# Optimization experiments

Measured on AMD Instinct MI355X. Metric: run time of the kernel, lower is better.

## Reference

```python
import jax, jax.numpy as jnp
import numpy as np

DIM = 256
N_STATE = 8
DT_RANK = 16  # ceil(dim/16)
D_CONV = 4
HIDDEN = 128  # dim * rank_ratio
EPS = 1e-6


def rmsnorm(x, w):
    # matches torch: x / (||x||_2 / sqrt(d) + eps) * w
    norm = jnp.sqrt(jnp.sum(x * x, axis=-1, keepdims=True))
    return x / (norm / np.sqrt(x.shape[-1]) + EPS) * w


def dwconv1d(x, w, b, pad_l, pad_r):
    # x: (b, l, c); w: (c, 1, k) depthwise
    out = jax.lax.conv_general_dilated(
        x.transpose(0, 2, 1), w, window_strides=(1,),
        padding=[(pad_l, pad_r)], dimension_numbers=('NCH', 'OIH', 'NCH'),
        feature_group_count=w.shape[0])
    return (out + b[None, :, None]).transpose(0, 2, 1)


def selective_scan(x, delta, A, Bm, Cm, D):
    # x, delta: (b,l,d); A: (d,n); Bm, Cm: (b,l,n); D: (d,)
    dA = jnp.exp(delta[..., None] * A)                     # (b,l,d,n)
    dBx = (delta * x)[..., None] * Bm[:, :, None, :]       # (b,l,d,n)

    def step(h, inp):
        dA_t, dBx_t, C_t = inp
        h = dA_t * h + dBx_t                               # (b,d,n)
        y = jnp.einsum('bdn,bn->bd', h, C_t)
        return h, y

    h0 = jnp.zeros((x.shape[0],) + A.shape, dtype=x.dtype)
    _, ys = jax.lax.scan(step, h0,
                         (dA.transpose(1, 0, 2, 3), dBx.transpose(1, 0, 2, 3),
                          Cm.transpose(1, 0, 2)))
    return ys.transpose(1, 0, 2) + x * D                   # (b,l,d)


def mamba_branch(x, ctx, conv_w, conv_b, xproj_w, dtproj_w, dtproj_b, A_log, D):
    xc = jax.nn.silu(dwconv1d(x, conv_w, conv_b, D_CONV - 1, 0))  # causal conv
    x_dbl = ctx @ xproj_w.T                                  # (b,l,r+2n)
    dt, Bm, Cm = jnp.split(x_dbl, [DT_RANK, DT_RANK + N_STATE], axis=-1)
    delta = jax.nn.softplus(dt @ dtproj_w.T + dtproj_b)
    A = -jnp.exp(A_log)
    return selective_scan(xc, delta, A, Bm, Cm, D)


def setup_inputs() -> dict:
    key = jax.random.key(0)
    ks = jax.random.split(key, 24)
    B, L, D = 4, 64 * 64, DIM
    s = 0.02
    A_log_init = jnp.log(jnp.broadcast_to(jnp.arange(1, N_STATE + 1, dtype=jnp.float32), (D, N_STATE)))
    dt_bias = jnp.full((D,), jnp.log(jnp.expm1(0.01)), dtype=jnp.float32)
    inp = {
        'x0': jax.random.normal(ks[0], (B, L, D), jnp.float32),
        'x1': jax.random.normal(ks[1], (B, L, D), jnp.float32),
        'w_norm0': jnp.ones((D,), jnp.float32),
        'w_norm1': jnp.ones((D,), jnp.float32),
        'in_proj_w': jax.random.normal(ks[2], (2 * D, D), jnp.float32) * s,
        'conv_w_f': jax.random.normal(ks[3], (D, 1, D_CONV), jnp.float32) * 0.3,
        'conv_b_f': jnp.zeros((D,), jnp.float32),
        'xproj_w_f': jax.random.normal(ks[4], (DT_RANK + 2 * N_STATE, D), jnp.float32) * s,
        'dtproj_w_f': jax.random.normal(ks[5], (D, DT_RANK), jnp.float32) * 0.1,
        'dtproj_b_f': dt_bias,
        'A_log_f': A_log_init,
        'D_f': jnp.ones((D,), jnp.float32),
        'conv_w_bw': jax.random.normal(ks[6], (D, 1, D_CONV), jnp.float32) * 0.3,
        'conv_b_bw': jnp.zeros((D,), jnp.float32),
        'xproj_w_bw': jax.random.normal(ks[7], (DT_RANK + 2 * N_STATE, D), jnp.float32) * s,
        'dtproj_w_bw': jax.random.normal(ks[8], (D, DT_RANK), jnp.float32) * 0.1,
        'dtproj_b_bw': dt_bias,
        'A_log_bw': A_log_init,
        'D_bw': jnp.ones((D,), jnp.float32),
        'norm_y_w': jnp.ones((D,), jnp.float32),
        'out_proj_w': jax.random.normal(ks[9], (D, D), jnp.float32) * s,
        'fc1_w': jax.random.normal(ks[10], (HIDDEN, D), jnp.float32) * s,
        'dw_w': jax.random.normal(ks[11], (HIDDEN, 1, 3), jnp.float32) * 0.3,
        'dw_b': jnp.zeros((HIDDEN,), jnp.float32),
        'fc2_w': jax.random.normal(ks[12], (D, HIDDEN), jnp.float32) * s,
    }
    return inp


def reference(x0, x1, w_norm0, w_norm1, in_proj_w, conv_w_f, conv_b_f, xproj_w_f,
              dtproj_w_f, dtproj_b_f, A_log_f, D_f, conv_w_bw, conv_b_bw,
              xproj_w_bw, dtproj_w_bw, dtproj_b_bw, A_log_bw, D_bw, norm_y_w,
              out_proj_w, fc1_w, dw_w, dw_b, fc2_w):
    residual = x0
    h0 = rmsnorm(x0, w_norm0)
    h1 = rmsnorm(x1, w_norm1)
    # cross-Mamba: main stream x0 -> x,z; extra_emb x1 -> dt/B/C
    xz = h0 @ in_proj_w.T
    xin, z = jnp.split(xz, 2, axis=-1)
    y_f = mamba_branch(xin, h1, conv_w_f, conv_b_f, xproj_w_f, dtproj_w_f,
                       dtproj_b_f, A_log_f, D_f)
    y_b = jnp.flip(mamba_branch(jnp.flip(xin, 1), jnp.flip(h1, 1), conv_w_bw,
                                conv_b_bw, xproj_w_bw, dtproj_w_bw, dtproj_b_bw,
                                A_log_bw, D_bw), 1)
    y = (y_f + y_b) * 0.5          # if_devide_out=True (bidirectional)
    y = rmsnorm(y, norm_y_w)       # use_norm=True
    y = y * jax.nn.silu(z)
    x = y @ out_proj_w.T + residual
    # LowRankFeedForward (dropout = identity at eval)
    m = x @ fc1_w.T
    m = jax.nn.silu(dwconv1d(m, dw_w, dw_b, 1, 1))
    m = m @ fc2_w.T
    return x + m
```

## Files before the change

kernel.cpp:

```cpp
#include <hip/hip_runtime.h>
#include <math.h>
#include <cstddef>

#define BB 4
#define LL 4096
#define DD 256
#define NST 8
#define RANK 16
#define HID 128
#define BL (BB*LL)
#define BLD ((size_t)BL*DD)
#define CH 256
#define CLEN 16
#define XZS 512

typedef __bf16 bf16x8 __attribute__((ext_vector_type(8)));
typedef float  f32x4  __attribute__((ext_vector_type(4)));

__device__ __forceinline__ float siluf(float x){ return x / (1.f + __expf(-x)); }
__device__ __forceinline__ float softplus_fast(float x){
  float r = __logf(1.f + __expf(x));
  return x > 15.f ? x : r;
}
__device__ __forceinline__ unsigned short f2bf(float x){
  union { float f; unsigned u; } v; v.f = x;
  unsigned r = v.u + 0x7fffu + ((v.u >> 16) & 1u);
  return (unsigned short)(r >> 16);
}
__device__ __forceinline__ float bf2f(unsigned short u){
  union { unsigned u32; float f; } c; c.u32 = ((unsigned)u) << 16;
  return c.f;
}

__global__ __launch_bounds__(64) void rms_kernel(
    const float* __restrict__ x0, const float* __restrict__ w0, unsigned short* __restrict__ o0b,
    const float* __restrict__ x1, const float* __restrict__ w1, unsigned short* __restrict__ o1b)
{
  const float* x; const float* w; unsigned short* o;
  if (blockIdx.y == 0){ x = x0; w = w0; o = o0b; } else { x = x1; w = w1; o = o1b; }
  size_t tok = blockIdx.x;
  int lane = threadIdx.x;
  float4 v = ((const float4*)(x + tok*DD))[lane];
  float s = v.x*v.x + v.y*v.y + v.z*v.z + v.w*v.w;
  #pragma unroll
  for (int m = 1; m < 64; m <<= 1) s += __shfl_xor(s, m, 64);
  float scale = 1.f / (sqrtf(s) * (1.f/16.f) + 1e-6f);
  float4 wv = ((const float4*)w)[lane];
  ushort4 r;
  r.x = f2bf(v.x*scale*wv.x); r.y = f2bf(v.y*scale*wv.y);
  r.z = f2bf(v.z*scale*wv.z); r.w = f2bf(v.w*scale*wv.w);
  ((ushort4*)(o + tok*DD))[lane] = r;
}

__global__ __launch_bounds__(256) void cvt1_kernel(
    const float* __restrict__ s, unsigned short* __restrict__ d, int n)
{
  int i = blockIdx.x*256 + threadIdx.x;
  if (i < n) d[i] = f2bf(s[i]);
}
__global__ __launch_bounds__(256) void cvt5_kernel(
    const float* __restrict__ s0, const float* __restrict__ s1,
    const float* __restrict__ s2, const float* __restrict__ s3,
    const float* __restrict__ s4, unsigned short* __restrict__ d)
{
  int i = blockIdx.x*256 + threadIdx.x;
  if (i >= 147456) return;
  float v;
  if (i < 8192)        v = s0[i];
  else if (i < 16384)  v = s1[i - 8192];
  else if (i < 81920)  v = s2[i - 16384];
  else if (i < 114688) v = s3[i - 81920];
  else                 v = s4[i - 114688];
  d[i] = f2bf(v);
}

template<int EPI>
__global__ __launch_bounds__(256) void gemm_mfma(
    const unsigned short* __restrict__ A, const unsigned short* __restrict__ Bw,
    float* __restrict__ C, const float* __restrict__ Add,
    unsigned short* __restrict__ Cb, int M, int ldc, int K)
{
  constexpr int BK = 64, PAD = 8;
  __shared__ __align__(16) unsigned short As[64][BK+PAD];
  __shared__ __align__(16) unsigned short Bs[64][BK+PAD];
  int tid  = threadIdx.x;
  int row0 = blockIdx.x * 64;
  int col0 = blockIdx.y * 64;
  int wave = tid >> 6, lane = tid & 63;
  int wm = (wave >> 1) * 32, wn = (wave & 1) * 32;
  int lm = lane & 15, kq = lane >> 4;
  int sr = tid >> 2, sc16 = (tid & 3) * 16;

  f32x4 acc[2][2];
  #pragma unroll
  for (int i = 0; i < 2; i++)
    #pragma unroll
    for (int j = 0; j < 2; j++) acc[i][j] = (f32x4){0.f,0.f,0.f,0.f};

  for (int k0 = 0; k0 < K; k0 += BK){
    const unsigned short* ap = &A [(size_t)(row0 + sr)*K + k0 + sc16];
    const unsigned short* bp = &Bw[(size_t)(col0 + sr)*K + k0 + sc16];
    *(int4*)&As[sr][sc16]   = *(const int4*)ap;
    *(int4*)&As[sr][sc16+8] = *(const int4*)(ap + 8);
    *(int4*)&Bs[sr][sc16]   = *(const int4*)bp;
    *(int4*)&Bs[sr][sc16+8] = *(const int4*)(bp + 8);
    __syncthreads();
    #pragma unroll
    for (int ks = 0; ks < 2; ks++){
      bf16x8 af[2], bfv[2];
      #pragma unroll
      for (int i = 0; i < 2; i++) af[i]  = *(const bf16x8*)&As[wm + i*16 + lm][ks*32 + kq*8];
      #pragma unroll
      for (int j = 0; j < 2; j++) bfv[j] = *(const bf16x8*)&Bs[wn + j*16 + lm][ks*32 + kq*8];
      #pragma unroll
      for (int i = 0; i < 2; i++)
        #pragma unroll
        for (int j = 0; j < 2; j++)
          acc[i][j] = __builtin_amdgcn_mfma_f32_16x16x32_bf16(af[i], bfv[j], acc[i][j], 0, 0, 0);
    }
    __syncthreads();
  }

  #pragma unroll
  for (int i = 0; i < 2; i++){
    int rbase = row0 + wm + i*16 + kq*4;
    #pragma unroll
    for (int j = 0; j < 2; j++){
      int col = col0 + wn + j*16 + lm;
      #pragma unroll
      for (int r = 0; r < 4; r++){
        size_t idx = (size_t)(rbase + r)*ldc + col;
        float v = acc[i][j][r];
        if constexpr (EPI == 1 || EPI == 2) v += Add[idx];
        if constexpr (EPI != 3) C[idx] = v;
        if constexpr (EPI == 1 || EPI == 3) Cb[idx] = f2bf(v);
      }
    }
  }
}

__global__ __launch_bounds__(256) void front_kernel(
    const unsigned short* __restrict__ xz,
    const float* __restrict__ xd,
    const float* __restrict__ cwf, const float* __restrict__ cbf,
    const float* __restrict__ cwb, const float* __restrict__ cbb,
    const float* __restrict__ dtwf, const float* __restrict__ dtbf,
    const float* __restrict__ dtwb, const float* __restrict__ dtbb,
    const float* __restrict__ Alogf, const float* __restrict__ Alogb,
    const float* __restrict__ Dfp, const float* __restrict__ Dbp,
    unsigned int* __restrict__ xde,
    float* __restrict__ Sp, float* __restrict__ Hout)
{
  int chunk = blockIdx.x, b = blockIdx.y, dir = blockIdx.z;
  int s0 = chunk*CLEN;
  int d  = threadIdx.x;

  __shared__ float sdt[CLEN][16];
  __shared__ float sB [CLEN][8];
  __shared__ float sC [CLEN][8];
  #pragma unroll
  for (int e = threadIdx.x; e < CLEN*32; e += 256){
    int lt = e >> 5, col = e & 31;
    int pos = s0 + lt;
    int row = dir ? (LL-1-pos) : pos;
    float v = xd[((size_t)b*LL + row)*64 + dir*32 + col];
    if (col < 16)      sdt[lt][col]    = v;
    else if (col < 24) sB [lt][col-16] = v;
    else               sC [lt][col-24] = v;
  }
  __syncthreads();

  float4 cw = ((const float4*)(dir ? cwb : cwf))[d];
  float cb  = (dir ? cbb : cbf)[d];
  const float* dtw = (dir ? dtwb : dtwf) + d*RANK;
  float4 w0 = ((const float4*)dtw)[0], w1 = ((const float4*)dtw)[1];
  float4 w2 = ((const float4*)dtw)[2], w3 = ((const float4*)dtw)[3];
  float dtb = (dir ? dtbb : dtbf)[d];
  float Dd  = (dir ? Dbp : Dfp)[d];

  const unsigned short* xp = xz + (size_t)b*LL*XZS + d;
  #define LDX(pos) ((pos) >= 0 ? bf2f(xp[(size_t)(dir ? (LL-1-(pos)) : (pos))*XZS]) : 0.f)

  float xv[CLEN+3];
  xv[0] = LDX(s0-3); xv[1] = LDX(s0-2); xv[2] = LDX(s0-1);
  #pragma unroll
  for (int i = 0; i < CLEN; i++) xv[3+i] = LDX(s0+i);
  #undef LDX

  unsigned packX[CLEN];
  #pragma unroll
  for (int i = 0; i < CLEN; i++){
    float xc = cb;
    xc = fmaf(cw.x, xv[i],   xc); xc = fmaf(cw.y, xv[i+1], xc);
    xc = fmaf(cw.z, xv[i+2], xc); xc = fmaf(cw.w, xv[i+3], xc);
    xc = siluf(xc);
    const float* dt = &sdt[i][0];
    float de = dtb;
    de = fmaf(dt[0],w0.x, fmaf(dt[1],w0.y, fmaf(dt[2],w0.z, fmaf(dt[3],w0.w, de))));
    de = fmaf(dt[4],w1.x, fmaf(dt[5],w1.y, fmaf(dt[6],w1.z, fmaf(dt[7],w1.w, de))));
    de = fmaf(dt[8],w2.x, fmaf(dt[9],w2.y, fmaf(dt[10],w2.z, fmaf(dt[11],w2.w, de))));
    de = fmaf(dt[12],w3.x, fmaf(dt[13],w3.y, fmaf(dt[14],w3.z, fmaf(dt[15],w3.w, de))));
    de = softplus_fast(de);
    packX[i] = (unsigned)f2bf(xc) | ((unsigned)f2bf(de) << 16);
  }

  const float* Alog = dir ? Alogb : Alogf;
  float A[NST];
  bool fast = true;
  #pragma unroll
  for (int n = 0; n < NST; n++){
    A[n] = -__expf(Alog[d*NST + n]);
    fast = fast && (fabsf(A[n] + (float)(n+1)) < 1e-3f);
  }
  float h[NST];
  #pragma unroll
  for (int n = 0; n < NST; n++) h[n] = 0.f;
  float S = 0.f;

  unsigned int* xout = xde + ((size_t)(dir*BB + b)*LL + s0)*DD + d;

  if (fast){
    #pragma unroll
    for (int t = 0; t < CLEN; t++){
      unsigned pk = packX[t];
      float xc = bf2f((unsigned short)(pk & 0xffffu));
      float de = bf2f((unsigned short)(pk >> 16));
      S += de;
      float dux = de * xc;
      const float* Bv = &sB[t][0];
      const float* Cv = &sC[t][0];
      float e1 = __expf(-de);
      float e2 = e1*e1, e3 = e2*e1, e4 = e2*e2;
      float e5 = e4*e1, e6 = e4*e2, e7 = e4*e3, e8 = e4*e4;
      float acc = xc * Dd;
      h[0] = fmaf(e1, h[0], dux*Bv[0]); acc = fmaf(h[0], Cv[0], acc);
      h[1] = fmaf(e2, h[1], dux*Bv[1]); acc = fmaf(h[1], Cv[1], acc);
      h[2] = fmaf(e3, h[2], dux*Bv[2]); acc = fmaf(h[2], Cv[2], acc);
      h[3] = fmaf(e4, h[3], dux*Bv[3]); acc = fmaf(h[3], Cv[3], acc);
      h[4] = fmaf(e5, h[4], dux*Bv[4]); acc = fmaf(h[4], Cv[4], acc);
      h[5] = fmaf(e6, h[5], dux*Bv[5]); acc = fmaf(h[5], Cv[5], acc);
      h[6] = fmaf(e7, h[6], dux*Bv[6]); acc = fmaf(h[6], Cv[6], acc);
      h[7] = fmaf(e8, h[7], dux*Bv[7]); acc = fmaf(h[7], Cv[7], acc);
      xout[(size_t)t*DD] = (pk & 0xffff0000u) | (unsigned)f2bf(acc);
    }
  } else {
    #pragma unroll
    for (int t = 0; t < CLEN; t++){
      unsigned pk = packX[t];
      float xc = bf2f((unsigned short)(pk & 0xffffu));
      float de = bf2f((unsigned short)(pk >> 16));
      S += de;
      float dux = de * xc;
      const float* Bv = &sB[t][0];
      const float* Cv = &sC[t][0];
      float acc = xc * Dd;
      #pragma unroll
      for (int n = 0; n < NST; n++){
        h[n] = fmaf(__expf(de*A[n]), h[n], dux*Bv[n]);
        acc = fmaf(h[n], Cv[n], acc);
      }
      xout[(size_t)t*DD] = (pk & 0xffff0000u) | (unsigned)f2bf(acc);
    }
  }

  size_t ob = ((((size_t)dir*CH + chunk)*BB + b)*DD + d)*NST;
  float4 h0v, h1v;
  h0v.x=h[0]; h0v.y=h[1]; h0v.z=h[2]; h0v.w=h[3];
  h1v.x=h[4]; h1v.y=h[5]; h1v.z=h[6]; h1v.w=h[7];
  *(float4*)&Hout[ob]   = h0v; *(float4*)&Hout[ob+4] = h1v;
  Sp[((size_t)(dir*CH + chunk)*BB + b)*DD + d] = S;
}

__global__ __launch_bounds__(64) void scan_p2(
    const float* __restrict__ Sp, float* H,
    const float* __restrict__ Alogf, const float* __restrict__ Alogb)
{
  const int SEGC = CH/8;
  int blk = blockIdx.x;
  int d   = blk & (DD-1);
  int b   = (blk >> 8) & (BB-1);
  int dir = blk >> 10;
  int t   = threadIdx.x;
  int seg = t >> 3, n = t & 7;
  float A = -__expf((dir ? Alogb : Alogf)[d*NST + n]);

  const size_t sstr = (size_t)BB*DD;
  const size_t hstr = (size_t)BB*DD*NST;
  size_t sb = (size_t)dir*CH*sstr + (size_t)b*DD + d;
  size_t hb = (size_t)dir*CH*hstr + ((size_t)b*DD + d)*NST + n;
  int c0 = seg*SEGC;

  float pv[SEGC], hv[SEGC];
  #pragma unroll
  for (int k = 0; k < SEGC; k++){
    pv[k] = Sp[sb + (size_t)(c0+k)*sstr];
    hv[k] = H [hb + (size_t)(c0+k)*hstr];
  }
  float h = 0.f, Ss = 0.f;
  #pragma unroll
  for (int k = 0; k < SEGC; k++){
    Ss += pv[k];
    pv[k] = __expf(pv[k]*A);
    h = fmaf(pv[k], h, hv[k]);
  }
  float pi = __expf(Ss*A), hi = h;
  #pragma unroll
  for (int off = 8; off < 64; off <<= 1){
    float hprev = __shfl_up(hi, off, 64);
    float pprev = __shfl_up(pi, off, 64);
    if (t >= off){ hi = fmaf(pi, hprev, hi); pi *= pprev; }
  }
  float hin = __shfl_up(hi, 8, 64);
  h = (seg == 0) ? 0.f : hin;
  #pragma unroll
  for (int k = 0; k < SEGC; k++){
    size_t idx = hb + (size_t)(c0+k)*hstr;
    H[idx] = h;
    h = fmaf(pv[k], h, hv[k]);
  }
}

__global__ __launch_bounds__(256) void back_kernel(
    const unsigned int* __restrict__ xde,
    const float* __restrict__ xd,
    const float* __restrict__ Alogf, const float* __restrict__ Alogb,
    const float* __restrict__ Hin,
    const unsigned short* __restrict__ xz,
    const float* __restrict__ wn,
    unsigned short* __restrict__ outb)
{
  int c  = blockIdx.x, b = blockIdx.y;
  int cbk = CH-1-c;
  int d  = threadIdx.x;
  int T0 = c*CLEN;
  int Pb = cbk*CLEN;

  __shared__ float sCf[CLEN][8], sCb[CLEN][8];
  __shared__ float red[CLEN][4];
  __shared__ float sscale[CLEN];
  {
    int k  = threadIdx.x & 7;
    int lt = (threadIdx.x >> 3) & 15;
    if (threadIdx.x < 128)
      sCf[lt][k] = xd[((size_t)b*LL + T0 + lt)*64 + 24 + k];
    else
      sCb[lt][k] = xd[((size_t)b*LL + (T0 + 15 - lt))*64 + 56 + k];
  }
  __syncthreads();

  float Af[NST], Ab[NST];
  bool fast = true;
  #pragma unroll
  for (int n = 0; n < NST; n++){
    Af[n] = -__expf(Alogf[d*NST + n]);
    Ab[n] = -__expf(Alogb[d*NST + n]);
    fast = fast && (fabsf(Af[n] + (float)(n+1)) < 1e-3f)
                && (fabsf(Ab[n] + (float)(n+1)) < 1e-3f);
  }

  float vf[CLEN];

  {
    float hn[NST];
    size_t ib = (((size_t)c*BB + b)*DD + d)*NST;
    float4 a0 = *(const float4*)&Hin[ib];
    float4 a1 = *(const float4*)&Hin[ib+4];
    hn[0]=a0.x; hn[1]=a0.y; hn[2]=a0.z; hn[3]=a0.w;
    hn[4]=a1.x; hn[5]=a1.y; hn[6]=a1.z; hn[7]=a1.w;
    const unsigned int* p = xde + ((size_t)b*LL + T0)*DD + d;
    unsigned int pk[CLEN];
    #pragma unroll
    for (int t = 0; t < CLEN; t++) pk[t] = p[(size_t)t*DD];
    float S = 0.f;
    if (fast){
      #pragma unroll
      for (int t = 0; t < CLEN; t++){
        float y0 = bf2f((unsigned short)(pk[t] & 0xffffu));
        float de = bf2f((unsigned short)(pk[t] >> 16));
        S += de;
        float E1 = __expf(-S);
        float E2 = E1*E1, E3 = E2*E1, E4 = E2*E2;
        float E5 = E4*E1, E6 = E4*E2, E7 = E4*E3, E8 = E4*E4;
        float corr =      E1 * (hn[0]*sCf[t][0]);
        corr = fmaf(E2, hn[1]*sCf[t][1], corr);
        corr = fmaf(E3, hn[2]*sCf[t][2], corr);
        corr = fmaf(E4, hn[3]*sCf[t][3], corr);
        corr = fmaf(E5, hn[4]*sCf[t][4], corr);
        corr = fmaf(E6, hn[5]*sCf[t][5], corr);
        corr = fmaf(E7, hn[6]*sCf[t][6], corr);
        corr = fmaf(E8, hn[7]*sCf[t][7], corr);
        vf[t] = y0 + corr;
      }
    } else {
      #pragma unroll
      for (int t = 0; t < CLEN; t++){
        float y0 = bf2f((unsigned short)(pk[t] & 0xffffu));
        float de = bf2f((unsigned short)(pk[t] >> 16));
        S += de;
        float corr = 0.f;
        #pragma unroll
        for (int n = 0; n < NST; n++)
          corr = fmaf(__expf(S*Af[n]), hn[n]*sCf[t][n], corr);
        vf[t] = y0 + corr;
      }
    }
  }

  {
    float hn[NST];
    size_t ib = ((((size_t)CH + cbk)*BB + b)*DD + d)*NST;
    float4 a0 = *(const float4*)&Hin[ib];
    float4 a1 = *(const float4*)&Hin[ib+4];
    hn[0]=a0.x; hn[1]=a0.y; hn[2]=a0.z; hn[3]=a0.w;
    hn[4]=a1.x; hn[5]=a1.y; hn[6]=a1.z; hn[7]=a1.w;
    const unsigned int* p = xde + ((size_t)(BB + b)*LL + Pb)*DD + d;
    unsigned int pk[CLEN];
    #pragma unroll
    for (int t = 0; t < CLEN; t++) pk[t] = p[(size_t)t*DD];
    float S = 0.f;
    if (fast){
      #pragma unroll
      for (int t = 0; t < CLEN; t++){
        float y0 = bf2f((unsigned short)(pk[t] & 0xffffu));
        float de = bf2f((unsigned short)(pk[t] >> 16));
        S += de;
        float E1 = __expf(-S);
        float E2 = E1*E1, E3 = E2*E1, E4 = E2*E2;
        float E5 = E4*E1, E6 = E4*E2, E7 = E4*E3, E8 = E4*E4;
        float corr =      E1 * (hn[0]*sCb[t][0]);
        corr = fmaf(E2, hn[1]*sCb[t][1], corr);
        corr = fmaf(E3, hn[2]*sCb[t][2], corr);
        corr = fmaf(E4, hn[3]*sCb[t][3], corr);
        corr = fmaf(E5, hn[4]*sCb[t][4], corr);
        corr = fmaf(E6, hn[5]*sCb[t][5], corr);
        corr = fmaf(E7, hn[6]*sCb[t][6], corr);
        corr = fmaf(E8, hn[7]*sCb[t][7], corr);
        int j = 15 - t;
        vf[j] = 0.5f*(vf[j] + y0 + corr);
      }
    } else {
      #pragma unroll
      for (int t = 0; t < CLEN; t++){
        float y0 = bf2f((unsigned short)(pk[t] & 0xffffu));
        float de = bf2f((unsigned short)(pk[t] >> 16));
        S += de;
        float corr = 0.f;
        #pragma unroll
        for (int n = 0; n < NST; n++)
          corr = fmaf(__expf(S*Ab[n]), hn[n]*sCb[t][n], corr);
        int j = 15 - t;
        vf[j] = 0.5f*(vf[j] + y0 + corr);
      }
    }
  }

  int wave = d >> 6, lane = d & 63;
  #pragma unroll
  for (int j = 0; j < CLEN; j++){
    float s = vf[j]*vf[j];
    #pragma unroll
    for (int m = 1; m < 64; m <<= 1) s += __shfl_xor(s, m, 64);
    if (lane == 0) red[j][wave] = s;
  }
  __syncthreads();
  if (d < CLEN){
    float s = red[d][0] + red[d][1] + red[d][2] + red[d][3];
    sscale[d] = 1.f / (sqrtf(s)*(1.f/16.f) + 1e-6f);
  }
  __syncthreads();

  float wd = wn[d];
  #pragma unroll
  for (int j = 0; j < CLEN; j++){
    size_t tok = (size_t)b*LL + T0 + j;
    float z = bf2f(xz[tok*XZS + 256 + d]);
    outb[tok*DD + d] = f2bf(vf[j]*sscale[j]*wd*siluf(z));
  }
}

__global__ __launch_bounds__(256) void dwconv3_kernel(
    const float* __restrict__ m, const float* __restrict__ w,
    const float* __restrict__ bi, unsigned short* __restrict__ o)
{
  size_t gid = (size_t)blockIdx.x*256 + threadIdx.x;
  int c = (int)(gid % HID);
  int tok = (int)(gid / HID);
  int b = tok / LL, t = tok % LL;
  float acc = bi[c];
  #pragma unroll
  for (int k = 0; k < 3; k++){
    int tt = t - 1 + k;
    if (tt >= 0 && tt < LL)
      acc = fmaf(w[c*3 + k], m[((size_t)b*LL + tt)*HID + c], acc);
  }
  o[gid] = f2bf(siluf(acc));
}

extern "C" void kernel_launch(void* const* d_in, const int* in_sizes, int n_in,
                              void* d_out, int out_size, void* d_ws, size_t ws_size,
                              hipStream_t stream)
{
  const float* x0        = (const float*)d_in[0];
  const float* x1        = (const float*)d_in[1];
  const float* w_norm0   = (const float*)d_in[2];
  const float* w_norm1   = (const float*)d_in[3];
  const float* in_proj_w = (const float*)d_in[4];
  const float* conv_w_f  = (const float*)d_in[5];
  const float* conv_b_f  = (const float*)d_in[6];
  const float* xproj_w_f = (const float*)d_in[7];
  const float* dtproj_w_f= (const float*)d_in[8];
  const float* dtproj_b_f= (const float*)d_in[9];
  const float* A_log_f   = (const float*)d_in[10];
  const float* D_f       = (const float*)d_in[11];
  const float* conv_w_bw = (const float*)d_in[12];
  const float* conv_b_bw = (const float*)d_in[13];
  const float* xproj_w_bw= (const float*)d_in[14];
  const float* dtproj_w_bw=(const float*)d_in[15];
  const float* dtproj_b_bw=(const float*)d_in[16];
  const float* A_log_bw  = (const float*)d_in[17];
  const float* D_bw      = (const float*)d_in[18];
  const float* norm_y_w  = (const float*)d_in[19];
  const float* out_proj_w= (const float*)d_in[20];
  const float* fc1_w     = (const float*)d_in[21];
  const float* dw_w      = (const float*)d_in[22];
  const float* dw_b      = (const float*)d_in[23];
  const float* fc2_w     = (const float*)d_in[24];
  float* out = (float*)d_out;
  float* ws  = (float*)d_ws;

  float* r0 = ws + 0*BLD;
  float* r1 = ws + 1*BLD;
  float* r2 = ws + 2*BLD;
  float* r3 = ws + 3*BLD;
  float* r4 = ws + 4*BLD;
  float* r5 = ws + 5*BLD;
  float* r6 = ws + 6*BLD;
  float* r7 = ws + 7*BLD;

  unsigned short* h0b   = (unsigned short*)r0;
  unsigned short* h1b   = (unsigned short*)r1;
  unsigned short* xz_b  = (unsigned short*)r2;
  float*          xd    = r3;
  unsigned int*   xde   = (unsigned int*)r4;
  unsigned short* wbuf1 = (unsigned short*)r6;
  float* Hout = r6;
  float* Hin  = Hout;
  const size_t SPLANE = (size_t)2*CH*BB*DD;
  float* Sp   = r7 + (BLD - SPLANE);
  unsigned short* ycomb_b = (unsigned short*)r0;
  unsigned short* wbuf2   = (unsigned short*)r7;
  unsigned short* wb_xp   = wbuf2;
  unsigned short* wb_out  = wbuf2 + 16384;
  unsigned short* wb_fc1  = wbuf2 + 81920;
  unsigned short* wb_fc2  = wbuf2 + 114688;
  unsigned short* xb      = wbuf2 + 147456;
  float*          m1      = r4;
  unsigned short* m2b     = (unsigned short*)r5;

  cvt1_kernel<<<dim3(512), 256, 0, stream>>>(in_proj_w, wbuf1, 131072);
  cvt5_kernel<<<dim3(576), 256, 0, stream>>>(
      xproj_w_f, xproj_w_bw, out_proj_w, fc1_w, fc2_w, wbuf2);

  rms_kernel<<<dim3(BL,2), 64, 0, stream>>>(x0, w_norm0, h0b, x1, w_norm1, h1b);

  gemm_mfma<3><<<dim3(BL/64, 8), 256, 0, stream>>>(
      h0b, wbuf1, nullptr, nullptr, xz_b, BL, XZS, 256);

  gemm_mfma<0><<<dim3(BL/64, 1), 256, 0, stream>>>(
      h1b, wb_xp, xd, nullptr, nullptr, BL, 64, 256);

  front_kernel<<<dim3(CH, BB, 2), 256, 0, stream>>>(
      xz_b, xd, conv_w_f, conv_b_f, conv_w_bw, conv_b_bw,
      dtproj_w_f, dtproj_b_f, dtproj_w_bw, dtproj_b_bw,
      A_log_f, A_log_bw, D_f, D_bw, xde, Sp, Hout);

  scan_p2<<<dim3(2*BB*DD), 64, 0, stream>>>(Sp, Hout, A_log_f, A_log_bw);

  back_kernel<<<dim3(CH, BB), 256, 0, stream>>>(
      xde, xd, A_log_f, A_log_bw, Hin, xz_b, norm_y_w, ycomb_b);

  gemm_mfma<1><<<dim3(BL/64, 4), 256, 0, stream>>>(
      ycomb_b, wb_out, out, x0, xb, BL, 256, 256);

  gemm_mfma<0><<<dim3(BL/64, 2), 256, 0, stream>>>(
      xb, wb_fc1, m1, nullptr, nullptr, BL, 128, 256);

  dwconv3_kernel<<<dim3((BL*HID)/256), 256, 0, stream>>>(m1, dw_w, dw_b, m2b);

  gemm_mfma<2><<<dim3(BL/64, 4), 256, 0, stream>>>(
      m2b, wb_fc2, out, out, nullptr, BL, 256, 128);
}
```

Before: 272.2 us.

## Merge weight conversion kernels, vectorize dwconv3, use running products for decay powers

Folds the two weight-conversion launches into one kernel to drop a launch. Vectorizes the depthwise conv3 kernel so each thread handles four channels, using float4 loads and ushort4 stores. Rewrites the decay-power computations in the scan kernels as a serial running product instead of a shallow product tree. The serial chain lengthens the dependency path in the scan's inner loops.

```diff
diff --git a/kernel.cpp b/kernel.cpp
--- a/kernel.cpp
+++ b/kernel.cpp
@@ -52,26 +52,24 @@
   ((ushort4*)(o + tok*DD))[lane] = r;
 }
 
-__global__ __launch_bounds__(256) void cvt1_kernel(
-    const float* __restrict__ s, unsigned short* __restrict__ d, int n)
-{
-  int i = blockIdx.x*256 + threadIdx.x;
-  if (i < n) d[i] = f2bf(s[i]);
-}
-__global__ __launch_bounds__(256) void cvt5_kernel(
+__global__ __launch_bounds__(256) void cvt_kernel(
+    const float* __restrict__ sA,
     const float* __restrict__ s0, const float* __restrict__ s1,
     const float* __restrict__ s2, const float* __restrict__ s3,
-    const float* __restrict__ s4, unsigned short* __restrict__ d)
+    const float* __restrict__ s4,
+    unsigned short* __restrict__ d1, unsigned short* __restrict__ d2)
 {
   int i = blockIdx.x*256 + threadIdx.x;
-  if (i >= 147456) return;
+  if (i >= 278528) return;
+  if (i < 131072){ d1[i] = f2bf(sA[i]); return; }
+  int j = i - 131072;
   float v;
-  if (i < 8192)        v = s0[i];
-  else if (i < 16384)  v = s1[i - 8192];
-  else if (i < 81920)  v = s2[i - 16384];
-  else if (i < 114688) v = s3[i - 81920];
-  else                 v = s4[i - 114688];
-  d[i] = f2bf(v);
+  if (j < 8192)        v = s0[j];
+  else if (j < 16384)  v = s1[j - 8192];
+  else if (j < 81920)  v = s2[j - 16384];
+  else if (j < 114688) v = s3[j - 81920];
+  else                 v = s4[j - 114688];
+  d2[j] = f2bf(v);
 }
 
 template<int EPI>
@@ -230,17 +228,16 @@
       const float* Bv = &sB[t][0];
       const float* Cv = &sC[t][0];
       float e1 = __expf(-de);
-      float e2 = e1*e1, e3 = e2*e1, e4 = e2*e2;
-      float e5 = e4*e1, e6 = e4*e2, e7 = e4*e3, e8 = e4*e4;
+      float dA = e1;
       float acc = xc * Dd;
-      h[0] = fmaf(e1, h[0], dux*Bv[0]); acc = fmaf(h[0], Cv[0], acc);
-      h[1] = fmaf(e2, h[1], dux*Bv[1]); acc = fmaf(h[1], Cv[1], acc);
-      h[2] = fmaf(e3, h[2], dux*Bv[2]); acc = fmaf(h[2], Cv[2], acc);
-      h[3] = fmaf(e4, h[3], dux*Bv[3]); acc = fmaf(h[3], Cv[3], acc);
-      h[4] = fmaf(e5, h[4], dux*Bv[4]); acc = fmaf(h[4], Cv[4], acc);
-      h[5] = fmaf(e6, h[5], dux*Bv[5]); acc = fmaf(h[5], Cv[5], acc);
-      h[6] = fmaf(e7, h[6], dux*Bv[6]); acc = fmaf(h[6], Cv[6], acc);
-      h[7] = fmaf(e8, h[7], dux*Bv[7]); acc = fmaf(h[7], Cv[7], acc);
+      h[0] = fmaf(dA, h[0], dux*Bv[0]); acc = fmaf(h[0], Cv[0], acc); dA *= e1;
+      h[1] = fmaf(dA, h[1], dux*Bv[1]); acc = fmaf(h[1], Cv[1], acc); dA *= e1;
+      h[2] = fmaf(dA, h[2], dux*Bv[2]); acc = fmaf(h[2], Cv[2], acc); dA *= e1;
+      h[3] = fmaf(dA, h[3], dux*Bv[3]); acc = fmaf(h[3], Cv[3], acc); dA *= e1;
+      h[4] = fmaf(dA, h[4], dux*Bv[4]); acc = fmaf(h[4], Cv[4], acc); dA *= e1;
+      h[5] = fmaf(dA, h[5], dux*Bv[5]); acc = fmaf(h[5], Cv[5], acc); dA *= e1;
+      h[6] = fmaf(dA, h[6], dux*Bv[6]); acc = fmaf(h[6], Cv[6], acc); dA *= e1;
+      h[7] = fmaf(dA, h[7], dux*Bv[7]); acc = fmaf(h[7], Cv[7], acc);
       xout[(size_t)t*DD] = (pk & 0xffff0000u) | (unsigned)f2bf(acc);
     }
   } else {
@@ -378,17 +375,16 @@
         float y0 = bf2f((unsigned short)(pk[t] & 0xffffu));
         float de = bf2f((unsigned short)(pk[t] >> 16));
         S += de;
-        float E1 = __expf(-S);
-        float E2 = E1*E1, E3 = E2*E1, E4 = E2*E2;
-        float E5 = E4*E1, E6 = E4*E2, E7 = E4*E3, E8 = E4*E4;
-        float corr =      E1 * (hn[0]*sCf[t][0]);
-        corr = fmaf(E2, hn[1]*sCf[t][1], corr);
-        corr = fmaf(E3, hn[2]*sCf[t][2], corr);
-        corr = fmaf(E4, hn[3]*sCf[t][3], corr);
-        corr = fmaf(E5, hn[4]*sCf[t][4], corr);
-        corr = fmaf(E6, hn[5]*sCf[t][5], corr);
-        corr = fmaf(E7, hn[6]*sCf[t][6], corr);
-        corr = fmaf(E8, hn[7]*sCf[t][7], corr);
+        float E = __expf(-S);
+        float q = E;
+        float corr = q * (hn[0]*sCf[t][0]);
+        q *= E; corr = fmaf(q, hn[1]*sCf[t][1], corr);
+        q *= E; corr = fmaf(q, hn[2]*sCf[t][2], corr);
+        q *= E; corr = fmaf(q, hn[3]*sCf[t][3], corr);
+        q *= E; corr = fmaf(q, hn[4]*sCf[t][4], corr);
+        q *= E; corr = fmaf(q, hn[5]*sCf[t][5], corr);
+        q *= E; corr = fmaf(q, hn[6]*sCf[t][6], corr);
+        q *= E; corr = fmaf(q, hn[7]*sCf[t][7], corr);
         vf[t] = y0 + corr;
       }
     } else {
@@ -424,17 +420,16 @@
         float y0 = bf2f((unsigned short)(pk[t] & 0xffffu));
         float de = bf2f((unsigned short)(pk[t] >> 16));
         S += de;
-        float E1 = __expf(-S);
-        float E2 = E1*E1, E3 = E2*E1, E4 = E2*E2;
-        float E5 = E4*E1, E6 = E4*E2, E7 = E4*E3, E8 = E4*E4;
-        float corr =      E1 * (hn[0]*sCb[t][0]);
-        corr = fmaf(E2, hn[1]*sCb[t][1], corr);
-        corr = fmaf(E3, hn[2]*sCb[t][2], corr);
-        corr = fmaf(E4, hn[3]*sCb[t][3], corr);
-        corr = fmaf(E5, hn[4]*sCb[t][4], corr);
-        corr = fmaf(E6, hn[5]*sCb[t][5], corr);
-        corr = fmaf(E7, hn[6]*sCb[t][6], corr);
-        corr = fmaf(E8, hn[7]*sCb[t][7], corr);
+        float E = __expf(-S);
+        float q = E;
+        float corr = q * (hn[0]*sCb[t][0]);
+        q *= E; corr = fmaf(q, hn[1]*sCb[t][1], corr);
+        q *= E; corr = fmaf(q, hn[2]*sCb[t][2], corr);
+        q *= E; corr = fmaf(q, hn[3]*sCb[t][3], corr);
+        q *= E; corr = fmaf(q, hn[4]*sCb[t][4], corr);
+        q *= E; corr = fmaf(q, hn[5]*sCb[t][5], corr);
+        q *= E; corr = fmaf(q, hn[6]*sCb[t][6], corr);
+        q *= E; corr = fmaf(q, hn[7]*sCb[t][7], corr);
         int j = 15 - t;
         vf[j] = 0.5f*(vf[j] + y0 + corr);
       }
@@ -483,17 +478,25 @@
     const float* __restrict__ bi, unsigned short* __restrict__ o)
 {
   size_t gid = (size_t)blockIdx.x*256 + threadIdx.x;
-  int c = (int)(gid % HID);
-  int tok = (int)(gid / HID);
-  int b = tok / LL, t = tok % LL;
-  float acc = bi[c];
+  int c4  = (int)(gid & 31) * 4;
+  int tok = (int)(gid >> 5);
+  int b = tok >> 12, t = tok & (LL-1);
+  float4 acc = {bi[c4], bi[c4+1], bi[c4+2], bi[c4+3]};
   #pragma unroll
   for (int k = 0; k < 3; k++){
     int tt = t - 1 + k;
-    if (tt >= 0 && tt < LL)
-      acc = fmaf(w[c*3 + k], m[((size_t)b*LL + tt)*HID + c], acc);
-  }
-  o[gid] = f2bf(siluf(acc));
+    if (tt >= 0 && tt < LL){
+      float4 mv = *(const float4*)&m[((size_t)b*LL + tt)*HID + c4];
+      acc.x = fmaf(w[c4*3 + k],       mv.x, acc.x);
+      acc.y = fmaf(w[(c4+1)*3 + k],   mv.y, acc.y);
+      acc.z = fmaf(w[(c4+2)*3 + k],   mv.z, acc.z);
+      acc.w = fmaf(w[(c4+3)*3 + k],   mv.w, acc.w);
+    }
+  }
+  ushort4 r;
+  r.x = f2bf(siluf(acc.x)); r.y = f2bf(siluf(acc.y));
+  r.z = f2bf(siluf(acc.z)); r.w = f2bf(siluf(acc.w));
+  *(ushort4*)&o[gid*4] = r;
 }
 
 extern "C" void kernel_launch(void* const* d_in, const int* in_sizes, int n_in,
@@ -557,9 +560,8 @@
   float*          m1      = r4;
   unsigned short* m2b     = (unsigned short*)r5;
 
-  cvt1_kernel<<<dim3(512), 256, 0, stream>>>(in_proj_w, wbuf1, 131072);
-  cvt5_kernel<<<dim3(576), 256, 0, stream>>>(
-      xproj_w_f, xproj_w_bw, out_proj_w, fc1_w, fc2_w, wbuf2);
+  cvt_kernel<<<dim3(1088), 256, 0, stream>>>(
+      in_proj_w, xproj_w_f, xproj_w_bw, out_proj_w, fc1_w, fc2_w, wbuf1, wbuf2);
 
   rms_kernel<<<dim3(BL,2), 64, 0, stream>>>(x0, w_norm0, h0b, x1, w_norm1, h1b);
 
@@ -585,7 +587,7 @@
   gemm_mfma<0><<<dim3(BL/64, 2), 256, 0, stream>>>(
       xb, wb_fc1, m1, nullptr, nullptr, BL, 128, 256);
 
-  dwconv3_kernel<<<dim3((BL*HID)/256), 256, 0, stream>>>(m1, dw_w, dw_b, m2b);
+  dwconv3_kernel<<<dim3((BL*HID/4)/256), 256, 0, stream>>>(m1, dw_w, dw_b, m2b);
 
   gemm_mfma<2><<<dim3(BL/64, 4), 256, 0, stream>>>(
       m2b, wb_fc2, out, out, nullptr, BL, 256, 128);
```

Result: faster. 261.0 us (-4.1%).
